# Kernel tuning notes

Hardware: AMD Instinct MI355X
Metric: run time of the kernel (lower is better)

## Reference

```python
import jax, jax.numpy as jnp
import numpy as np


def setup_inputs() -> dict:
    key = jax.random.key(0)
    k1, k2, k3, k4 = jax.random.split(key, 4)
    L, d, n_tokens = 4096, 2048, 4096
    x = jax.random.normal(k1, (L, d), dtype=jnp.float32)
    Wq_w = jax.random.normal(k2, (d, d), dtype=jnp.float32) * (1.0 / np.sqrt(d))
    Pk = jax.random.normal(k3, (1, n_tokens, d), dtype=jnp.float32)
    Pv = jax.random.normal(k4, (1, n_tokens, d), dtype=jnp.float32)
    return {"x": x, "Wq_w": Wq_w, "Pk": Pk, "Pv": Pv, "sliding_window_size": 1024}


def reference(x, Wq_w, Pk, Pv, sliding_window_size):
    # x: (L, d); Pk/Pv: (1, n_tokens, d). Single-head cross attention to a
    # fixed parameter token bank with a bidirectional sliding-window mask
    # |q_idx - kv_idx| < sliding_window_size (flex_attention semantics,
    # default scale = 1/sqrt(d)).
    L, d = x.shape
    n_tokens = Pk.shape[1]
    scale = 1.0 / np.sqrt(d).astype(np.float32)

    q = x @ Wq_w.T                                    # (L, d)
    scores = jnp.einsum('ld,td->lt', q, Pk[0]) * scale  # (L, n_tokens)

    q_idx = jnp.arange(L)[:, None]
    kv_idx = jnp.arange(n_tokens)[None, :]
    mask = jnp.abs(q_idx - kv_idx) < sliding_window_size  # (L, n_tokens)

    neg_inf = jnp.asarray(jnp.finfo(scores.dtype).min, scores.dtype)
    probs = jax.nn.softmax(jnp.where(mask, scores, neg_inf), axis=-1)
    y = jnp.einsum('lt,td->ld', probs, Pv[0])         # (L, d)
    return y[None, :, :]                              # (1, L, d) after squeeze(1)
```

## Files before the change

kernel.cpp:

```cpp
#include <hip/hip_runtime.h>


using bf16x8 = __attribute__((ext_vector_type(8))) short;
using f32x4  = __attribute__((ext_vector_type(4))) float;

#define LDIM 4096
#define TDIM 4096
#define DDIM 2048

#define HBUF 8192

static __device__ __forceinline__ unsigned short f2bf(float f) {
  union { float f; unsigned u; } c; c.f = f;
  unsigned r = c.u + 0x7FFFu + ((c.u >> 16) & 1u);
  return (unsigned short)(r >> 16);
}
static __device__ __forceinline__ unsigned pack2(float a, float b) {
  return (unsigned)f2bf(a) | ((unsigned)f2bf(b) << 16);
}
static __device__ __forceinline__ void gload16(const void* g, void* l) {
  __builtin_amdgcn_global_load_lds((const __attribute__((address_space(1))) void*)g,
                                   (__attribute__((address_space(3))) void*)l, 16, 0, 0);
}

__global__ __launch_bounds__(256) void k_prep(const float* __restrict__ x,
                                              const float* __restrict__ Wq,
                                              const float* __restrict__ Pk,
                                              const float* __restrict__ Pv,
                                              unsigned short* __restrict__ xb,
                                              unsigned short* __restrict__ wb,
                                              unsigned short* __restrict__ kb,
                                              unsigned short* __restrict__ vt,
                                              float* __restrict__ rowsum) {
  const int tid = threadIdx.x;
  const int b = blockIdx.x;
  if (b < 10240) {
    const float* in; unsigned short* out; size_t i;
    if (b < 4096)      { in = x;  out = xb; i = (size_t)b * 256 + tid; }
    else if (b < 6144) { in = Wq; out = wb; i = (size_t)(b - 4096) * 256 + tid; }
    else               { in = Pk; out = kb; i = (size_t)(b - 6144) * 256 + tid; }
    const float4* p = (const float4*)(in + i * 8);
    float4 a = p[0], c = p[1];
    uint4 o = { pack2(a.x, a.y), pack2(a.z, a.w), pack2(c.x, c.y), pack2(c.z, c.w) };
    *(uint4*)(out + i * 8) = o;
    return;
  }
  if (b == 12288) {
    for (int k = tid; k < LDIM; k += 256) rowsum[k] = 0.f;
    return;
  }
  __shared__ unsigned short tile[64][72];
  const int b2 = b - 10240;
  const int t0 = (b2 & 63) * 64, j0 = (b2 >> 6) * 64;
  const int r = tid >> 4, c4 = (tid & 15) * 4;
#pragma unroll
  for (int rr = 0; rr < 64; rr += 16) {
    float4 v = *(const float4*)(Pv + (size_t)(t0 + r + rr) * DDIM + j0 + c4);
    tile[c4 + 0][r + rr] = f2bf(v.x);
    tile[c4 + 1][r + rr] = f2bf(v.y);
    tile[c4 + 2][r + rr] = f2bf(v.z);
    tile[c4 + 3][r + rr] = f2bf(v.w);
  }
  __syncthreads();
  const int jr = tid >> 3, tc = (tid & 7) * 8;
#pragma unroll
  for (int jj = 0; jj < 64; jj += 32)
    *(uint4*)(vt + (size_t)(j0 + jr + jj) * TDIM + t0 + tc) =
        *(const uint4*)&tile[jr + jj][tc];
}

static __device__ __forceinline__ void gemm_loop(const unsigned short* __restrict__ A,
                                                 const unsigned short* __restrict__ B,
                                                 int m0, int n0, long lda, long ldb,
                                                 int kbeg, int kend,
                                                 unsigned short* As, unsigned short* Bs,
                                                 f32x4 (&acc)[4][2]) {
  const int tid = threadIdx.x;
  const int wave = tid >> 6, lane = tid & 63;
  const int quad = lane >> 4, l16 = lane & 15;
  const int wm = wave >> 2, wn = wave & 3;
  const int srow = wave * 16 + (lane >> 3);
  const int scb  = (lane & 7) ^ (lane >> 3);

  const unsigned short* gA = A + (long)(m0 + srow) * lda + scb * 8;
  const unsigned short* gB = B + (long)(n0 + srow) * ldb + scb * 8;
  unsigned short* lA = As + wave * 1024;
  unsigned short* lB = Bs + wave * 1024;

  const int sw = (l16 & 7) * 8;

#define STAGE(k0, bo) do {                                    \
    gload16(gA + (k0),           lA + (bo));                  \
    gload16(gA + (k0) + 8 * lda, lA + (bo) + 512);            \
    gload16(gB + (k0),           lB + (bo));                  \
    gload16(gB + (k0) + 8 * ldb, lB + (bo) + 512); } while (0)

#define COMPUTE(bo) do {                                                          \
    bf16x8 af[4][2], bfr[2][2];                                                   \
    _Pragma("unroll")                                                             \
    for (int i = 0; i < 4; i++)                                                   \
      _Pragma("unroll")                                                           \
      for (int h = 0; h < 2; h++)                                                 \
        af[i][h] = *(const bf16x8*)&As[(bo) + (wm * 64 + i * 16 + l16) * 64 +     \
                                       (((h * 4 + quad) * 8) ^ sw)];              \
    _Pragma("unroll")                                                             \
    for (int j = 0; j < 2; j++)                                                   \
      _Pragma("unroll")                                                           \
      for (int h = 0; h < 2; h++)                                                 \
        bfr[j][h] = *(const bf16x8*)&Bs[(bo) + (wn * 32 + j * 16 + l16) * 64 +    \
                                        (((h * 4 + quad) * 8) ^ sw)];             \
    _Pragma("unroll")                                                             \
    for (int h = 0; h < 2; h++)                                                   \
      _Pragma("unroll")                                                           \
      for (int i = 0; i < 4; i++)                                                 \
        _Pragma("unroll")                                                         \
        for (int j = 0; j < 2; j++)                                               \
          acc[i][j] = __builtin_amdgcn_mfma_f32_16x16x32_bf16(af[i][h], bfr[j][h],\
                                                              acc[i][j], 0, 0, 0);\
  } while (0)

  STAGE(kbeg, 0);
  __syncthreads();
  for (int k0 = kbeg; k0 < kend; k0 += 128) {
    STAGE(k0 + 64, HBUF);
    COMPUTE(0);
    __syncthreads();
    if (k0 + 128 < kend) STAGE(k0 + 128, 0);
    COMPUTE(HBUF);
    __syncthreads();
  }
#undef STAGE
#undef COMPUTE
}

__global__ __launch_bounds__(512) void k1_qgemm(const unsigned short* __restrict__ X,
                                                const unsigned short* __restrict__ W,
                                                unsigned short* __restrict__ q) {
  __shared__ __align__(16) unsigned short As[2 * HBUF];
  __shared__ __align__(16) unsigned short Bs[2 * HBUF];
  const unsigned flat = blockIdx.y * 16 + blockIdx.x;
  const unsigned swz = (flat & 7) * 64 + (flat >> 3);
  const int bx = swz & 15, by = swz >> 4;
  f32x4 acc[4][2] = {};
  const int m0 = by * 128, n0 = bx * 128;
  gemm_loop(X, W, m0, n0, DDIM, DDIM, 0, DDIM, As, Bs, acc);
  const int tid = threadIdx.x;
  const int wave = tid >> 6, lane = tid & 63;
  const int quad = lane >> 4, l16 = lane & 15, wm = wave >> 2, wn = wave & 3;
#pragma unroll
  for (int i = 0; i < 4; i++)
#pragma unroll
    for (int j = 0; j < 2; j++)
#pragma unroll
      for (int r = 0; r < 4; r++) {
        int row = m0 + wm * 64 + i * 16 + quad * 4 + r;
        int col = n0 + wn * 32 + j * 16 + l16;
        q[(long)row * DDIM + col] = f2bf(acc[i][j][r]);
      }
}

__global__ __launch_bounds__(512) void k2_qk(const unsigned short* __restrict__ Q,
                                             const unsigned short* __restrict__ Kb,
                                             unsigned short* __restrict__ P,
                                             float* __restrict__ rowsum,
                                             const int* __restrict__ wptr) {
  const unsigned flat = blockIdx.y * 32 + blockIdx.x;
  const unsigned swz = (flat & 7) * 128 + (flat >> 3);
  const int bx = swz & 31, by = swz >> 5;
  const int w = *wptr;
  const int l0 = by * 128, t0 = bx * 128;
  int lo = l0 - w + 1; if (lo < 0) lo = 0;
  int hi = l0 + 127 + w - 1; if (hi > TDIM - 1) hi = TDIM - 1;
  if (bx < (lo >> 7) || bx > (hi >> 7)) return;
  __shared__ __align__(16) unsigned short As[2 * HBUF];
  __shared__ __align__(16) unsigned short Bs[2 * HBUF];
  f32x4 acc[4][2] = {};
  gemm_loop(Q, Kb, l0, t0, DDIM, DDIM, 0, DDIM, As, Bs, acc);
  const float scale = 0.022097086912079608f;
  const int tid = threadIdx.x;
  const int wave = tid >> 6, lane = tid & 63;
  const int quad = lane >> 4, l16 = lane & 15, wm = wave >> 2, wn = wave & 3;
#pragma unroll
  for (int i = 0; i < 4; i++) {
    float rs[4] = {0.f, 0.f, 0.f, 0.f};
#pragma unroll
    for (int j = 0; j < 2; j++)
#pragma unroll
      for (int r = 0; r < 4; r++) {
        int l = l0 + wm * 64 + i * 16 + quad * 4 + r;
        int t = t0 + wn * 32 + j * 16 + l16;
        int dlt = l - t; dlt = dlt < 0 ? -dlt : dlt;
        float e = 0.f;
        if (dlt < w) e = __expf(acc[i][j][r] * scale);
        unsigned short bv = f2bf(e);
        P[(long)l * TDIM + t] = bv;
        rs[r] += __uint_as_float((unsigned)bv << 16);
      }
#pragma unroll
    for (int r = 0; r < 4; ++r) {
      float s = rs[r];
      s += __shfl_xor(s, 1);
      s += __shfl_xor(s, 2);
      s += __shfl_xor(s, 4);
      s += __shfl_xor(s, 8);
      if (l16 == 0) atomicAdd(&rowsum[l0 + wm * 64 + i * 16 + quad * 4 + r], s);
    }
  }
}

__global__ __launch_bounds__(512) void k3_pv(const unsigned short* __restrict__ P,
                                             const unsigned short* __restrict__ Vt,
                                             const float* __restrict__ rowsum,
                                             float* __restrict__ Y,
                                             const int* __restrict__ wptr) {
  const unsigned flat = blockIdx.y * 16 + blockIdx.x;
  const unsigned swz = (flat & 7) * 64 + (flat >> 3);
  const int bx = swz & 15, by = swz >> 4;
  const int w = *wptr;
  const int l0 = by * 128, j0 = bx * 128;
  int lo = l0 - w + 1; if (lo < 0) lo = 0;
  int hi = l0 + 127 + w - 1; if (hi > TDIM - 1) hi = TDIM - 1;
  const int kb = (lo >> 7) * 128, ke = ((hi >> 7) + 1) * 128;
  __shared__ __align__(16) unsigned short As[2 * HBUF];
  __shared__ __align__(16) unsigned short Bs[2 * HBUF];
  f32x4 acc[4][2] = {};
  gemm_loop(P, Vt, l0, j0, TDIM, TDIM, kb, ke, As, Bs, acc);
  const int tid = threadIdx.x;
  const int wave = tid >> 6, lane = tid & 63;
  const int quad = lane >> 4, l16 = lane & 15, wm = wave >> 2, wn = wave & 3;
#pragma unroll
  for (int i = 0; i < 4; i++)
#pragma unroll
    for (int r = 0; r < 4; r++) {
      const int l = l0 + wm * 64 + i * 16 + quad * 4 + r;
      const float inv = 1.0f / rowsum[l];
#pragma unroll
      for (int j = 0; j < 2; j++)
        Y[(long)l * DDIM + j0 + wn * 32 + j * 16 + l16] = acc[i][j][r] * inv;
    }
}

extern "C" void kernel_launch(void* const* d_in, const int* in_sizes, int n_in,
                              void* d_out, int out_size, void* d_ws, size_t ws_size,
                              hipStream_t stream) {
  const float* x  = (const float*)d_in[0];
  const float* Wq = (const float*)d_in[1];
  const float* Pk = (const float*)d_in[2];
  const float* Pv = (const float*)d_in[3];
  const int* wptr = (const int*)d_in[4];
  float* Y = (float*)d_out;

  unsigned short* base = (unsigned short*)d_ws;
  unsigned short* Pm = base;
  unsigned short* xb = base;
  unsigned short* wb = base + (size_t)LDIM * DDIM;
  unsigned short* kb = base + (size_t)TDIM * TDIM;
  unsigned short* vt = kb + (size_t)TDIM * DDIM;
  unsigned short* qb = vt + (size_t)DDIM * TDIM;
  float* rowsum = (float*)(qb + (size_t)LDIM * DDIM);

  k_prep<<<12289, 256, 0, stream>>>(x, Wq, Pk, Pv, xb, wb, kb, vt, rowsum);
  k1_qgemm<<<dim3(DDIM / 128, LDIM / 128), 512, 0, stream>>>(xb, wb, qb);
  k2_qk<<<dim3(TDIM / 128, LDIM / 128), 512, 0, stream>>>(qb, kb, Pm, rowsum, wptr);
  k3_pv<<<dim3(DDIM / 128, LDIM / 128), 512, 0, stream>>>(Pm, vt, rowsum, Y, wptr);
}
```

Measured before the change: 306.1 us.

## Halve GEMM K-stage to 32 and replace syncthreads with vmcnt waits plus barriers

Shrinks the per-stage K chunk of the shared bf16 GEMM loop from 64 to 32 and halves the LDS double buffer, with a new XOR swizzle for the 32-wide rows. The loop is restructured to use explicit s_waitcnt vmcnt(0) plus s_barrier once per half-step, with a peeled tail, instead of two __syncthreads. The aim is to cut LDS footprint, which may allow higher occupancy, and lighter synchronisation. In exchange there are twice as many barriers per unit of K and less MFMA work between each sync.

```diff
diff --git a/kernel.cpp b/kernel.cpp
--- a/kernel.cpp
+++ b/kernel.cpp
@@ -8,7 +8,7 @@
 #define TDIM 4096
 #define DDIM 2048
 
-#define HBUF 8192
+#define HBUF 4096
 
 static __device__ __forceinline__ unsigned short f2bf(float f) {
   union { float f; unsigned u; } c; c.f = f;
@@ -79,56 +79,56 @@
   const int wave = tid >> 6, lane = tid & 63;
   const int quad = lane >> 4, l16 = lane & 15;
   const int wm = wave >> 2, wn = wave & 3;
-  const int srow = wave * 16 + (lane >> 3);
-  const int scb  = (lane & 7) ^ (lane >> 3);
+  const int srow = wave * 16 + (lane >> 2);
+  const int scb  = (lane & 3) ^ ((lane >> 3) & 3);
 
   const unsigned short* gA = A + (long)(m0 + srow) * lda + scb * 8;
   const unsigned short* gB = B + (long)(n0 + srow) * ldb + scb * 8;
-  unsigned short* lA = As + wave * 1024;
-  unsigned short* lB = Bs + wave * 1024;
-
-  const int sw = (l16 & 7) * 8;
-
-#define STAGE(k0, bo) do {                                    \
-    gload16(gA + (k0),           lA + (bo));                  \
-    gload16(gA + (k0) + 8 * lda, lA + (bo) + 512);            \
-    gload16(gB + (k0),           lB + (bo));                  \
-    gload16(gB + (k0) + 8 * ldb, lB + (bo) + 512); } while (0)
-
-#define COMPUTE(bo) do {                                                          \
-    bf16x8 af[4][2], bfr[2][2];                                                   \
-    _Pragma("unroll")                                                             \
-    for (int i = 0; i < 4; i++)                                                   \
-      _Pragma("unroll")                                                           \
-      for (int h = 0; h < 2; h++)                                                 \
-        af[i][h] = *(const bf16x8*)&As[(bo) + (wm * 64 + i * 16 + l16) * 64 +     \
-                                       (((h * 4 + quad) * 8) ^ sw)];              \
-    _Pragma("unroll")                                                             \
-    for (int j = 0; j < 2; j++)                                                   \
-      _Pragma("unroll")                                                           \
-      for (int h = 0; h < 2; h++)                                                 \
-        bfr[j][h] = *(const bf16x8*)&Bs[(bo) + (wn * 32 + j * 16 + l16) * 64 +    \
-                                        (((h * 4 + quad) * 8) ^ sw)];             \
-    _Pragma("unroll")                                                             \
-    for (int h = 0; h < 2; h++)                                                   \
-      _Pragma("unroll")                                                           \
-      for (int i = 0; i < 4; i++)                                                 \
-        _Pragma("unroll")                                                         \
-        for (int j = 0; j < 2; j++)                                               \
-          acc[i][j] = __builtin_amdgcn_mfma_f32_16x16x32_bf16(af[i][h], bfr[j][h],\
-                                                              acc[i][j], 0, 0, 0);\
+  unsigned short* lA = As + wave * 512;
+  unsigned short* lB = Bs + wave * 512;
+
+  const int kx = (quad ^ ((l16 >> 1) & 3)) * 8;
+
+#define STAGE(k0, bo) do {                 \
+    gload16(gA + (k0), lA + (bo));         \
+    gload16(gB + (k0), lB + (bo)); } while (0)
+
+#define COMPUTE(bo) do {                                                           \
+    bf16x8 af[4], bfr[2];                                                          \
+    _Pragma("unroll")                                                              \
+    for (int i = 0; i < 4; i++)                                                    \
+      af[i] = *(const bf16x8*)&As[(bo) + (wm * 64 + i * 16 + l16) * 32 + kx];      \
+    _Pragma("unroll")                                                              \
+    for (int j = 0; j < 2; j++)                                                    \
+      bfr[j] = *(const bf16x8*)&Bs[(bo) + (wn * 32 + j * 16 + l16) * 32 + kx];     \
+    _Pragma("unroll")                                                              \
+    for (int i = 0; i < 4; i++)                                                    \
+      _Pragma("unroll")                                                            \
+      for (int j = 0; j < 2; j++)                                                  \
+        acc[i][j] = __builtin_amdgcn_mfma_f32_16x16x32_bf16(af[i], bfr[j],         \
+                                                            acc[i][j], 0, 0, 0);   \
   } while (0)
 
   STAGE(kbeg, 0);
-  __syncthreads();
-  for (int k0 = kbeg; k0 < kend; k0 += 128) {
-    STAGE(k0 + 64, HBUF);
+  const int np = (kend - kbeg) >> 6;
+  int k0 = kbeg;
+  for (int p = 0; p < np - 1; ++p, k0 += 64) {
+    asm volatile("s_waitcnt vmcnt(0)" ::: "memory");
+    __builtin_amdgcn_s_barrier();
+    STAGE(k0 + 32, HBUF);
     COMPUTE(0);
-    __syncthreads();
-    if (k0 + 128 < kend) STAGE(k0 + 128, 0);
+    asm volatile("s_waitcnt vmcnt(0)" ::: "memory");
+    __builtin_amdgcn_s_barrier();
+    STAGE(k0 + 64, 0);
     COMPUTE(HBUF);
-    __syncthreads();
-  }
+  }
+  asm volatile("s_waitcnt vmcnt(0)" ::: "memory");
+  __builtin_amdgcn_s_barrier();
+  STAGE(k0 + 32, HBUF);
+  COMPUTE(0);
+  asm volatile("s_waitcnt vmcnt(0)" ::: "memory");
+  __builtin_amdgcn_s_barrier();
+  COMPUTE(HBUF);
 #undef STAGE
 #undef COMPUTE
 }
```

Measured after the change: 307.6 us. Within noise of the previous version (+0.5%).
